# Optimization experiments

Measured on AMD Instinct MI355X. Metric: run time of the kernel, lower is better.

## Reference

```python
import jax, jax.numpy as jnp
import numpy as np

QMAX = 127.0          # int8 clip bound (symmetric, preserve-zero)
QDIV = 127.5          # AQT int8 scale divisor: 2**(bits-1) - 0.5


def _safe(s):
    # avoid div-by-zero for all-zero rows/cols
    return jnp.where(s == 0.0, 1.0, s)


def setup_inputs() -> dict:
    key = jax.random.key(0)
    k1, k2 = jax.random.split(key)
    lhs = jax.random.normal(k1, (8192, 4096), dtype=jnp.float32)
    rhs = jax.random.normal(k2, (4096, 4096), dtype=jnp.float32)
    return {"lhs": lhs, "rhs": rhs}


def reference(lhs, rhs):
    # --- dynamic symmetric int8 quantization (AQT abs-max calibration) ---
    # lhs: contract over axis 1 -> per-row scale [M, 1]
    s_l = _safe(jnp.max(jnp.abs(lhs), axis=1, keepdims=True) / QDIV)
    # rhs: contract over axis 0 -> per-column scale [1, N]
    s_r = _safe(jnp.max(jnp.abs(rhs), axis=0, keepdims=True) / QDIV)

    q_l = jnp.clip(jnp.round(lhs / s_l), -QMAX, QMAX).astype(jnp.int8)
    q_r = jnp.clip(jnp.round(rhs / s_r), -QMAX, QMAX).astype(jnp.int8)

    # --- integer matmul with int32 accumulation ---
    acc = jax.lax.dot_general(
        q_l, q_r,
        dimension_numbers=(((1,), (0,)), ((), ())),
        preferred_element_type=jnp.int32,
    )

    # --- dequantize: outer product of per-row / per-column scales ---
    return acc.astype(jnp.float32) * s_l * s_r
```

## Files before the change

### kernel.cpp

```cpp
#include <hip/hip_runtime.h>
#include <stdint.h>

#define M_DIM 8192
#define N_DIM 4096
#define K_DIM 4096
#define QMAXF 127.0f
#define QDIVF 127.5f

typedef int v4i __attribute__((ext_vector_type(4)));

typedef __attribute__((address_space(3))) void lds_void_t;
typedef __attribute__((address_space(1))) const void glb_void_t;

static __device__ __forceinline__ void load_lds16(const void* g, void* l) {
    __builtin_amdgcn_global_load_lds((glb_void_t*)g, (lds_void_t*)l, 16, 0, 0);
}

__global__ __launch_bounds__(256) void prep1_kernel(
        const float* __restrict__ lhs, const float* __restrict__ rhs,
        float* __restrict__ sL, unsigned* __restrict__ bits,
        int8_t* __restrict__ ql) {
    const int t = threadIdx.x;
    if (blockIdx.x < M_DIM) {
        const int row = blockIdx.x;
        const float4* rp = (const float4*)(lhs + (size_t)row * K_DIM);
        float4 v[4];
        float m = 0.0f;
#pragma unroll
        for (int i = 0; i < 4; ++i) {
            v[i] = rp[t + i * 256];
            m = fmaxf(m, fmaxf(fmaxf(fabsf(v[i].x), fabsf(v[i].y)),
                               fmaxf(fabsf(v[i].z), fabsf(v[i].w))));
        }
#pragma unroll
        for (int off = 32; off; off >>= 1) m = fmaxf(m, __shfl_down(m, off, 64));
        __shared__ float wmax[4];
        if ((t & 63) == 0) wmax[t >> 6] = m;
        __syncthreads();
        const float mm = fmaxf(fmaxf(wmax[0], wmax[1]), fmaxf(wmax[2], wmax[3]));
        float s = mm / QDIVF;
        s = (s == 0.0f) ? 1.0f : s;
        if (t == 0) sL[row] = s;
        unsigned* qo = (unsigned*)ql + (size_t)row * 1024;
#pragma unroll
        for (int i = 0; i < 4; ++i) {
            int q0 = (int)fminf(fmaxf(rintf(v[i].x / s), -QMAXF), QMAXF);
            int q1 = (int)fminf(fmaxf(rintf(v[i].y / s), -QMAXF), QMAXF);
            int q2 = (int)fminf(fmaxf(rintf(v[i].z / s), -QMAXF), QMAXF);
            int q3 = (int)fminf(fmaxf(rintf(v[i].w / s), -QMAXF), QMAXF);
            qo[t + i * 256] = (q0 & 255) | ((q1 & 255) << 8) | ((q2 & 255) << 16)
                            | ((unsigned)(q3 & 255) << 24);
        }
    } else {
        const int cb = blockIdx.x - M_DIM;
        const int col = (cb & 15) * 256 + t;
        const int r0 = (cb >> 4) * 64;
        float m = 0.0f;
#pragma unroll 4
        for (int r = 0; r < 64; ++r)
            m = fmaxf(m, fabsf(rhs[(size_t)(r0 + r) * N_DIM + col]));
        atomicMax(&bits[col], __float_as_uint(m));
    }
}

__global__ __launch_bounds__(256) void quant_rhs_t_kernel(
        const float* __restrict__ rhs, const unsigned* __restrict__ bits,
        float* __restrict__ sR, int8_t* __restrict__ qbT) {
    __shared__ __align__(16) int8_t lt[64][80];
    const int n0 = blockIdx.x * 64;
    const int k0 = blockIdx.y * 64;
    const int t = threadIdx.x;
    const int nloc = t & 63;
    const int kq = (t >> 6) * 16;
    float s = __uint_as_float(bits[n0 + nloc]) / QDIVF;
    s = (s == 0.0f) ? 1.0f : s;
    if (blockIdx.y == 0 && t < 64) {
        float ss = __uint_as_float(bits[n0 + t]) / QDIVF;
        sR[n0 + t] = (ss == 0.0f) ? 1.0f : ss;
    }
#pragma unroll
    for (int i = 0; i < 4; ++i) {
        unsigned pack = 0;
#pragma unroll
        for (int j = 0; j < 4; ++j) {
            int kk = kq + i * 4 + j;
            float x = rhs[(size_t)(k0 + kk) * N_DIM + n0 + nloc];
            int q = (int)fminf(fmaxf(rintf(x / s), -QMAXF), QMAXF);
            pack |= (unsigned)(q & 255) << (8 * j);
        }
        *(unsigned*)&lt[nloc][kq + i * 4] = pack;
    }
    __syncthreads();
    const int nn = t >> 2, ch = t & 3;
    v4i val = *(const v4i*)&lt[nn][ch * 16];
    *(v4i*)&qbT[(size_t)(n0 + nn) * K_DIM + k0 + ch * 16] = val;
}


#define BAR() do { asm volatile("" ::: "memory");          \
                   __builtin_amdgcn_s_barrier();           \
                   asm volatile("" ::: "memory"); } while (0)

#define VMCNT(N) asm volatile("s_waitcnt vmcnt(%0)" :: "n"(N) : "memory")

#define TILE(KT, BUF, S, VM) do {                                               \
    if (S) {                                                                    \
        load_lds16(gA0 + (size_t)((KT) + 2) * 64,                               \
                   lds + (((BUF) + 2) % 3) * 24576 + sdst);                     \
        load_lds16(gB0 + (size_t)((KT) + 2) * 64,                               \
                   lds + (((BUF) + 2) % 3) * 24576 + 8192 + sdst);              \
        load_lds16(gB0 + (size_t)128 * K_DIM + (size_t)((KT) + 2) * 64,         \
                   lds + (((BUF) + 2) % 3) * 24576 + 16384 + sdst);             \
    }                                                                           \
    _Pragma("unroll") for (int mm = 0; mm < 4; ++mm)                            \
        af[mm] = *(const v4i*)(lds + (BUF) * 24576 + aoff[mm]);                 \
    _Pragma("unroll") for (int nn = 0; nn < 4; ++nn)                            \
        bf[nn] = *(const v4i*)(lds + (BUF) * 24576 + boff[nn]);                 \
    __builtin_amdgcn_s_setprio(1);                                              \
    _Pragma("unroll") for (int mm = 0; mm < 4; ++mm)                            \
    _Pragma("unroll") for (int nn = 0; nn < 4; ++nn)                            \
        acc[mm][nn] = __builtin_amdgcn_mfma_i32_16x16x64_i8(                    \
            af[mm], bf[nn], acc[mm][nn], 0, 0, 0);                              \
    __builtin_amdgcn_s_setprio(0);                                              \
    VMCNT(VM);                                                                  \
    BAR();                                                                      \
} while (0)

__global__ __launch_bounds__(512, 4) void gemm_i8_kernel(
        const int8_t* __restrict__ qa, const int8_t* __restrict__ qbT,
        const float* __restrict__ sL, const float* __restrict__ sR,
        float* __restrict__ out) {
    __shared__ __align__(16) int8_t lds[73728];

    const int t = threadIdx.x;
    const int wave = t >> 6;
    const int lane = t & 63;

    const int bid = blockIdx.x;
    const int xcd = bid & 7;
    const int idx = bid >> 3;
    const int mt = (xcd >> 1) * 16 + (idx & 15);
    const int nt = (xcd & 1) * 8 + (idx >> 4);
    const int brow = mt * 128;
    const int bcol = nt * 256;

    const int wm = (wave >> 2) * 64;
    const int wn = (wave & 3) * 64;

    int aoff[4], boff[4];
#pragma unroll
    for (int m = 0; m < 4; ++m) {
        int row = wm + m * 16 + (lane & 15);
        aoff[m] = row * 64 + (((lane >> 4) ^ ((row >> 1) & 3)) * 16);
    }
#pragma unroll
    for (int n = 0; n < 4; ++n) {
        int row = wn + n * 16 + (lane & 15);
        boff[n] = 8192 + row * 64 + (((lane >> 4) ^ ((row >> 1) & 3)) * 16);
    }

    v4i acc[4][4];
#pragma unroll
    for (int m = 0; m < 4; ++m)
#pragma unroll
        for (int n = 0; n < 4; ++n) acc[m][n] = (v4i){0, 0, 0, 0};

    const int srow = t >> 2;
    const int lcA = (t & 3) ^ ((srow >> 1) & 3);
    const int8_t* gA0 = qa  + (size_t)(brow + srow) * K_DIM + lcA * 16;
    const int8_t* gB0 = qbT + (size_t)(bcol + srow) * K_DIM + lcA * 16;
    const int sdst = t * 16;

    v4i af[4], bf[4];

    load_lds16(gA0,                        lds + sdst);
    load_lds16(gB0,                        lds + 8192 + sdst);
    load_lds16(gB0 + (size_t)128 * K_DIM,  lds + 16384 + sdst);
    load_lds16(gA0 + 64,                       lds + 24576 + sdst);
    load_lds16(gB0 + 64,                       lds + 24576 + 8192 + sdst);
    load_lds16(gB0 + (size_t)128 * K_DIM + 64, lds + 24576 + 16384 + sdst);
    VMCNT(3);
    BAR();

    for (int kt = 0; kt < 60; kt += 3) {
        TILE(kt + 0, 0, 1, 3);
        TILE(kt + 1, 1, 1, 3);
        TILE(kt + 2, 2, 1, 3);
    }
    TILE(60, 0, 1, 3);
    TILE(61, 1, 1, 3);
    TILE(62, 2, 0, 0);
    TILE(63, 0, 0, 0);

    const int r4 = (lane >> 4) * 4;
    const int cc = lane & 15;
#pragma unroll
    for (int m = 0; m < 4; ++m) {
        const int grow0 = brow + wm + m * 16 + r4;
        const float s0 = sL[grow0 + 0];
        const float s1 = sL[grow0 + 1];
        const float s2 = sL[grow0 + 2];
        const float s3 = sL[grow0 + 3];
#pragma unroll
        for (int n = 0; n < 4; ++n) {
            const int gcol = bcol + wn + n * 16 + cc;
            const float sc = sR[gcol];
            float* o = out + (size_t)grow0 * N_DIM + gcol;
            o[0 * N_DIM] = (float)acc[m][n][0] * s0 * sc;
            o[1 * N_DIM] = (float)acc[m][n][1] * s1 * sc;
            o[2 * N_DIM] = (float)acc[m][n][2] * s2 * sc;
            o[3 * N_DIM] = (float)acc[m][n][3] * s3 * sc;
        }
    }
}

extern "C" void kernel_launch(void* const* d_in, const int* in_sizes, int n_in,
                              void* d_out, int out_size, void* d_ws, size_t ws_size,
                              hipStream_t stream) {
    const float* lhs = (const float*)d_in[0];
    const float* rhs = (const float*)d_in[1];
    float* out = (float*)d_out;

    uint8_t* ws = (uint8_t*)d_ws;
    int8_t* ql    = (int8_t*)ws;
    int8_t* qbT   = (int8_t*)(ws + 33554432);
    float* sL     = (float*)(ws + 50331648);
    float* sR     = (float*)(ws + 50331648 + 32768);
    unsigned* bits = (unsigned*)(ws + 50331648 + 32768 + 16384);

    hipMemsetAsync(bits, 0, N_DIM * sizeof(unsigned), stream);

    prep1_kernel<<<M_DIM + 1024, 256, 0, stream>>>(lhs, rhs, sL, bits, ql);
    quant_rhs_t_kernel<<<dim3(N_DIM / 64, K_DIM / 64), 256, 0, stream>>>(
        rhs, bits, sR, qbT);
    gemm_i8_kernel<<<dim3((M_DIM / 128) * (N_DIM / 256)), 512, 0, stream>>>(
        ql, qbT, sL, sR, out);
}
```

Before: 223.7 us.

## Enlarge GEMM tile to 256x256, load A fragments directly into registers

The int8 GEMM block tile grows from 128x256 to 256x256, and each wave now computes 64x128 with 32 accumulators. The A operand no longer goes through LDS: each wave loads its A fragments straight from global memory into double-buffered registers one k-step ahead. B stays staged in a 4-deep LDS ring via global_load_lds. This halves the grid and raises per-block reuse, in exchange for much higher register pressure (occupancy bound lowered to 2), and it relies on uncoalesced per-lane global A loads being hidden by the prefetch.

```diff
diff --git a/kernel.cpp b/kernel.cpp
--- a/kernel.cpp
+++ b/kernel.cpp
@@ -103,34 +103,34 @@
 
 #define VMCNT(N) asm volatile("s_waitcnt vmcnt(%0)" :: "n"(N) : "memory")
 
-#define TILE(KT, BUF, S, VM) do {                                               \
-    if (S) {                                                                    \
-        load_lds16(gA0 + (size_t)((KT) + 2) * 64,                               \
-                   lds + (((BUF) + 2) % 3) * 24576 + sdst);                     \
+#define TILE(KT, BUF, PAR, SA, SB, VM) do {                                     \
+    if (SA) {                                                                   \
+        _Pragma("unroll") for (int mm = 0; mm < 4; ++mm)                        \
+            an[(PAR) ^ 1][mm] = *(const v4i*)(pa[mm] + ((KT) + 1) * 64);        \
+    }                                                                           \
+    if (SB) {                                                                   \
         load_lds16(gB0 + (size_t)((KT) + 2) * 64,                               \
-                   lds + (((BUF) + 2) % 3) * 24576 + 8192 + sdst);              \
+                   lds + (((KT) + 2) & 3) * 16384 + sdst);                      \
         load_lds16(gB0 + (size_t)128 * K_DIM + (size_t)((KT) + 2) * 64,         \
-                   lds + (((BUF) + 2) % 3) * 24576 + 16384 + sdst);             \
+                   lds + (((KT) + 2) & 3) * 16384 + 8192 + sdst);               \
     }                                                                           \
-    _Pragma("unroll") for (int mm = 0; mm < 4; ++mm)                            \
-        af[mm] = *(const v4i*)(lds + (BUF) * 24576 + aoff[mm]);                 \
-    _Pragma("unroll") for (int nn = 0; nn < 4; ++nn)                            \
-        bf[nn] = *(const v4i*)(lds + (BUF) * 24576 + boff[nn]);                 \
+    _Pragma("unroll") for (int nn = 0; nn < 8; ++nn)                            \
+        bf[nn] = *(const v4i*)(lds + (BUF) * 16384 + boff[nn]);                 \
     __builtin_amdgcn_s_setprio(1);                                              \
     _Pragma("unroll") for (int mm = 0; mm < 4; ++mm)                            \
-    _Pragma("unroll") for (int nn = 0; nn < 4; ++nn)                            \
+    _Pragma("unroll") for (int nn = 0; nn < 8; ++nn)                            \
         acc[mm][nn] = __builtin_amdgcn_mfma_i32_16x16x64_i8(                    \
-            af[mm], bf[nn], acc[mm][nn], 0, 0, 0);                              \
+            an[PAR][mm], bf[nn], acc[mm][nn], 0, 0, 0);                         \
     __builtin_amdgcn_s_setprio(0);                                              \
     VMCNT(VM);                                                                  \
     BAR();                                                                      \
 } while (0)
 
-__global__ __launch_bounds__(512, 4) void gemm_i8_kernel(
+__global__ __launch_bounds__(512, 2) void gemm_i8_kernel(
         const int8_t* __restrict__ qa, const int8_t* __restrict__ qbT,
         const float* __restrict__ sL, const float* __restrict__ sR,
         float* __restrict__ out) {
-    __shared__ __align__(16) int8_t lds[73728];
+    __shared__ __align__(16) int8_t lds[65536];
 
     const int t = threadIdx.x;
     const int wave = t >> 6;
@@ -139,58 +139,59 @@
     const int bid = blockIdx.x;
     const int xcd = bid & 7;
     const int idx = bid >> 3;
-    const int mt = (xcd >> 1) * 16 + (idx & 15);
-    const int nt = (xcd & 1) * 8 + (idx >> 4);
-    const int brow = mt * 128;
+    const int mt = (xcd >> 1) * 8 + (idx >> 3);
+    const int nt = (xcd & 1) * 8 + (idx & 7);
+    const int brow = mt * 256;
     const int bcol = nt * 256;
 
-    const int wm = (wave >> 2) * 64;
-    const int wn = (wave & 3) * 64;
-
-    int aoff[4], boff[4];
-#pragma unroll
-    for (int m = 0; m < 4; ++m) {
-        int row = wm + m * 16 + (lane & 15);
-        aoff[m] = row * 64 + (((lane >> 4) ^ ((row >> 1) & 3)) * 16);
-    }
-#pragma unroll
-    for (int n = 0; n < 4; ++n) {
+    const int wm = (wave >> 1) * 64;
+    const int wn = (wave & 1) * 128;
+
+    const int8_t* pa[4];
+#pragma unroll
+    for (int m = 0; m < 4; ++m)
+        pa[m] = qa + (size_t)(brow + wm + m * 16 + (lane & 15)) * K_DIM
+                   + (lane >> 4) * 16;
+
+    int boff[8];
+#pragma unroll
+    for (int n = 0; n < 8; ++n) {
         int row = wn + n * 16 + (lane & 15);
-        boff[n] = 8192 + row * 64 + (((lane >> 4) ^ ((row >> 1) & 3)) * 16);
-    }
-
-    v4i acc[4][4];
+        boff[n] = row * 64 + (((lane >> 4) ^ ((row >> 1) & 3)) * 16);
+    }
+
+    v4i acc[4][8];
 #pragma unroll
     for (int m = 0; m < 4; ++m)
 #pragma unroll
-        for (int n = 0; n < 4; ++n) acc[m][n] = (v4i){0, 0, 0, 0};
+        for (int n = 0; n < 8; ++n) acc[m][n] = (v4i){0, 0, 0, 0};
 
     const int srow = t >> 2;
     const int lcA = (t & 3) ^ ((srow >> 1) & 3);
-    const int8_t* gA0 = qa  + (size_t)(brow + srow) * K_DIM + lcA * 16;
     const int8_t* gB0 = qbT + (size_t)(bcol + srow) * K_DIM + lcA * 16;
     const int sdst = t * 16;
 
-    v4i af[4], bf[4];
-
-    load_lds16(gA0,                        lds + sdst);
-    load_lds16(gB0,                        lds + 8192 + sdst);
-    load_lds16(gB0 + (size_t)128 * K_DIM,  lds + 16384 + sdst);
-    load_lds16(gA0 + 64,                       lds + 24576 + sdst);
-    load_lds16(gB0 + 64,                       lds + 24576 + 8192 + sdst);
-    load_lds16(gB0 + (size_t)128 * K_DIM + 64, lds + 24576 + 16384 + sdst);
-    VMCNT(3);
+    v4i an[2][4], bf[8];
+
+    load_lds16(gB0,                             lds + sdst);
+    load_lds16(gB0 + (size_t)128 * K_DIM,       lds + 8192 + sdst);
+    load_lds16(gB0 + 64,                        lds + 16384 + sdst);
+    load_lds16(gB0 + (size_t)128 * K_DIM + 64,  lds + 16384 + 8192 + sdst);
+#pragma unroll
+    for (int mm = 0; mm < 4; ++mm) an[0][mm] = *(const v4i*)(pa[mm]);
+    VMCNT(6);
     BAR();
 
-    for (int kt = 0; kt < 60; kt += 3) {
-        TILE(kt + 0, 0, 1, 3);
-        TILE(kt + 1, 1, 1, 3);
-        TILE(kt + 2, 2, 1, 3);
-    }
-    TILE(60, 0, 1, 3);
-    TILE(61, 1, 1, 3);
-    TILE(62, 2, 0, 0);
-    TILE(63, 0, 0, 0);
+    for (int kt = 0; kt < 60; kt += 4) {
+        TILE(kt + 0, 0, 0, 1, 1, 6);
+        TILE(kt + 1, 1, 1, 1, 1, 6);
+        TILE(kt + 2, 2, 0, 1, 1, 6);
+        TILE(kt + 3, 3, 1, 1, 1, 6);
+    }
+    TILE(60, 0, 0, 1, 1, 6);
+    TILE(61, 1, 1, 1, 1, 6);
+    TILE(62, 2, 0, 1, 0, 4);
+    TILE(63, 3, 1, 0, 0, 0);
 
     const int r4 = (lane >> 4) * 4;
     const int cc = lane & 15;
@@ -202,7 +203,7 @@
         const float s2 = sL[grow0 + 2];
         const float s3 = sL[grow0 + 3];
 #pragma unroll
-        for (int n = 0; n < 4; ++n) {
+        for (int n = 0; n < 8; ++n) {
             const int gcol = bcol + wn + n * 16 + cc;
             const float sc = sR[gcol];
             float* o = out + (size_t)grow0 * N_DIM + gcol;
@@ -233,6 +234,6 @@
     prep1_kernel<<<M_DIM + 1024, 256, 0, stream>>>(lhs, rhs, sL, bits, ql);
     quant_rhs_t_kernel<<<dim3(N_DIM / 64, K_DIM / 64), 256, 0, stream>>>(
         rhs, bits, sR, qbT);
-    gemm_i8_kernel<<<dim3((M_DIM / 128) * (N_DIM / 256)), 512, 0, stream>>>(
+    gemm_i8_kernel<<<dim3((M_DIM / 256) * (N_DIM / 256)), 512, 0, stream>>>(
         ql, qbT, sL, sR, out);
 }
```

Result: slower. 263.1 us (+17.6%).

## Enlarge GEMM tile to 256x256 with 8-phase interleaved LDS staging

Applied to the files above, without the earlier changes.

Doubles the block tile along M to 256x256, so each wave computes a 128x64 sub-tile with 32 accumulators. Each k-step is split into four phases, each issuing one quarter of the next stage's global-to-LDS loads before a chunk of MFMAs, with barriers between phases. The aim is more data reuse per byte loaded and better overlap of loads with compute. In exchange it uses more LDS (96KB) and more accumulator registers, lowers occupancy to 2 blocks, launches half as many blocks, and adds many extra barriers per k-step.

```diff
diff --git a/kernel.cpp b/kernel.cpp
--- a/kernel.cpp
+++ b/kernel.cpp
@@ -103,34 +103,51 @@
 
 #define VMCNT(N) asm volatile("s_waitcnt vmcnt(%0)" :: "n"(N) : "memory")
 
-#define TILE(KT, BUF, S, VM) do {                                               \
-    if (S) {                                                                    \
-        load_lds16(gA0 + (size_t)((KT) + 2) * 64,                               \
-                   lds + (((BUF) + 2) % 3) * 24576 + sdst);                     \
-        load_lds16(gB0 + (size_t)((KT) + 2) * 64,                               \
-                   lds + (((BUF) + 2) % 3) * 24576 + 8192 + sdst);              \
-        load_lds16(gB0 + (size_t)128 * K_DIM + (size_t)((KT) + 2) * 64,         \
-                   lds + (((BUF) + 2) % 3) * 24576 + 16384 + sdst);             \
-    }                                                                           \
+#define RD_A(BUF, MF) (*(const v4i*)(lds + (BUF) * 32768 + aoff[MF]))
+#define RD_B(BUF, NF) (*(const v4i*)(lds + (BUF) * 32768 + boff[NF]))
+
+#define STAGE_H(PTR, KT, OFF) \
+    load_lds16((PTR) + (size_t)(KT) * 64, lds + ((KT) % 3) * 32768 + (OFF) + sdst8)
+
+#define MFMA8(MB, NB)                                                           \
     _Pragma("unroll") for (int mm = 0; mm < 4; ++mm)                            \
-        af[mm] = *(const v4i*)(lds + (BUF) * 24576 + aoff[mm]);                 \
-    _Pragma("unroll") for (int nn = 0; nn < 4; ++nn)                            \
-        bf[nn] = *(const v4i*)(lds + (BUF) * 24576 + boff[nn]);                 \
-    __builtin_amdgcn_s_setprio(1);                                              \
-    _Pragma("unroll") for (int mm = 0; mm < 4; ++mm)                            \
-    _Pragma("unroll") for (int nn = 0; nn < 4; ++nn)                            \
-        acc[mm][nn] = __builtin_amdgcn_mfma_i32_16x16x64_i8(                    \
-            af[mm], bf[nn], acc[mm][nn], 0, 0, 0);                              \
-    __builtin_amdgcn_s_setprio(0);                                              \
-    VMCNT(VM);                                                                  \
+    _Pragma("unroll") for (int nn = 0; nn < 2; ++nn)                            \
+        acc[(MB) + mm][(NB) + nn] = __builtin_amdgcn_mfma_i32_16x16x64_i8(      \
+            af[mm], bf[(NB) + nn], acc[(MB) + mm][(NB) + nn], 0, 0, 0);
+
+#define TILE8(KT, BUF, S, VMLAST) do {                                          \
+                                                              \
+    _Pragma("unroll") for (int mm = 0; mm < 4; ++mm) af[mm] = RD_A(BUF, mm);    \
+    bf[0] = RD_B(BUF, 0); bf[1] = RD_B(BUF, 1);                                 \
+    if (S) STAGE_H(gA0, (KT) + 2, 0);                                           \
+    BAR();                                                                      \
+    __builtin_amdgcn_s_setprio(1); MFMA8(0, 0); __builtin_amdgcn_s_setprio(0);  \
+    BAR();                                                                      \
+                                                              \
+    bf[2] = RD_B(BUF, 2); bf[3] = RD_B(BUF, 3);                                 \
+    if (S) STAGE_H(gA1, (KT) + 2, 8192);                                        \
+    BAR();                                                                      \
+    __builtin_amdgcn_s_setprio(1); MFMA8(0, 2); __builtin_amdgcn_s_setprio(0);  \
+    BAR();                                                                      \
+                                                              \
+    _Pragma("unroll") for (int mm = 0; mm < 4; ++mm) af[mm] = RD_A(BUF, 4 + mm);\
+    if (S) STAGE_H(gB0, (KT) + 2, 16384);                                       \
+    BAR();                                                                      \
+    __builtin_amdgcn_s_setprio(1); MFMA8(4, 0); __builtin_amdgcn_s_setprio(0);  \
+    BAR();                                                                      \
+                                                              \
+    if (S) STAGE_H(gB1, (KT) + 2, 24576);                                       \
+    VMCNT(VMLAST);                                                              \
+    BAR();                                                                      \
+    __builtin_amdgcn_s_setprio(1); MFMA8(4, 2); __builtin_amdgcn_s_setprio(0);  \
     BAR();                                                                      \
 } while (0)
 
-__global__ __launch_bounds__(512, 4) void gemm_i8_kernel(
+__global__ __launch_bounds__(512, 2) void gemm_i8_kernel(
         const int8_t* __restrict__ qa, const int8_t* __restrict__ qbT,
         const float* __restrict__ sL, const float* __restrict__ sR,
         float* __restrict__ out) {
-    __shared__ __align__(16) int8_t lds[73728];
+    __shared__ __align__(16) int8_t lds[98304];
 
     const int t = threadIdx.x;
     const int wave = t >> 6;
@@ -139,63 +156,63 @@
     const int bid = blockIdx.x;
     const int xcd = bid & 7;
     const int idx = bid >> 3;
-    const int mt = (xcd >> 1) * 16 + (idx & 15);
-    const int nt = (xcd & 1) * 8 + (idx >> 4);
-    const int brow = mt * 128;
+    const int mt = (xcd >> 1) * 8 + (idx & 7);
+    const int nt = (xcd & 1) * 8 + (idx >> 3);
+    const int brow = mt * 256;
     const int bcol = nt * 256;
 
-    const int wm = (wave >> 2) * 64;
+    const int wm = (wave >> 2) * 128;
     const int wn = (wave & 3) * 64;
 
-    int aoff[4], boff[4];
-#pragma unroll
-    for (int m = 0; m < 4; ++m) {
+    int aoff[8], boff[4];
+#pragma unroll
+    for (int m = 0; m < 8; ++m) {
         int row = wm + m * 16 + (lane & 15);
         aoff[m] = row * 64 + (((lane >> 4) ^ ((row >> 1) & 3)) * 16);
     }
 #pragma unroll
     for (int n = 0; n < 4; ++n) {
         int row = wn + n * 16 + (lane & 15);
-        boff[n] = 8192 + row * 64 + (((lane >> 4) ^ ((row >> 1) & 3)) * 16);
-    }
-
-    v4i acc[4][4];
-#pragma unroll
-    for (int m = 0; m < 4; ++m)
+        boff[n] = 16384 + row * 64 + (((lane >> 4) ^ ((row >> 1) & 3)) * 16);
+    }
+
+    v4i acc[8][4];
+#pragma unroll
+    for (int m = 0; m < 8; ++m)
 #pragma unroll
         for (int n = 0; n < 4; ++n) acc[m][n] = (v4i){0, 0, 0, 0};
 
     const int srow = t >> 2;
     const int lcA = (t & 3) ^ ((srow >> 1) & 3);
     const int8_t* gA0 = qa  + (size_t)(brow + srow) * K_DIM + lcA * 16;
+    const int8_t* gA1 = gA0 + (size_t)128 * K_DIM;
     const int8_t* gB0 = qbT + (size_t)(bcol + srow) * K_DIM + lcA * 16;
-    const int sdst = t * 16;
+    const int8_t* gB1 = gB0 + (size_t)128 * K_DIM;
+    const int sdst8 = t * 16;
 
     v4i af[4], bf[4];
 
-    load_lds16(gA0,                        lds + sdst);
-    load_lds16(gB0,                        lds + 8192 + sdst);
-    load_lds16(gB0 + (size_t)128 * K_DIM,  lds + 16384 + sdst);
-    load_lds16(gA0 + 64,                       lds + 24576 + sdst);
-    load_lds16(gB0 + 64,                       lds + 24576 + 8192 + sdst);
-    load_lds16(gB0 + (size_t)128 * K_DIM + 64, lds + 24576 + 16384 + sdst);
-    VMCNT(3);
+    STAGE_H(gA0, 0, 0); STAGE_H(gA1, 0, 8192);
+    STAGE_H(gB0, 0, 16384); STAGE_H(gB1, 0, 24576);
+    STAGE_H(gA0, 1, 0); STAGE_H(gA1, 1, 8192);
+    STAGE_H(gB0, 1, 16384); STAGE_H(gB1, 1, 24576);
+    VMCNT(4);
     BAR();
 
     for (int kt = 0; kt < 60; kt += 3) {
-        TILE(kt + 0, 0, 1, 3);
-        TILE(kt + 1, 1, 1, 3);
-        TILE(kt + 2, 2, 1, 3);
-    }
-    TILE(60, 0, 1, 3);
-    TILE(61, 1, 1, 3);
-    TILE(62, 2, 0, 0);
-    TILE(63, 0, 0, 0);
+        TILE8(kt + 0, 0, 1, 4);
+        TILE8(kt + 1, 1, 1, 4);
+        TILE8(kt + 2, 2, 1, 4);
+    }
+    TILE8(60, 0, 1, 4);
+    TILE8(61, 1, 1, 4);
+    TILE8(62, 2, 0, 0);
+    TILE8(63, 0, 0, 0);
 
     const int r4 = (lane >> 4) * 4;
     const int cc = lane & 15;
 #pragma unroll
-    for (int m = 0; m < 4; ++m) {
+    for (int m = 0; m < 8; ++m) {
         const int grow0 = brow + wm + m * 16 + r4;
         const float s0 = sL[grow0 + 0];
         const float s1 = sL[grow0 + 1];
@@ -233,6 +250,6 @@
     prep1_kernel<<<M_DIM + 1024, 256, 0, stream>>>(lhs, rhs, sL, bits, ql);
     quant_rhs_t_kernel<<<dim3(N_DIM / 64, K_DIM / 64), 256, 0, stream>>>(
         rhs, bits, sR, qbT);
-    gemm_i8_kernel<<<dim3((M_DIM / 128) * (N_DIM / 256)), 512, 0, stream>>>(
+    gemm_i8_kernel<<<dim3((M_DIM / 256) * (N_DIM / 256)), 512, 0, stream>>>(
         ql, qbT, sL, sR, out);
 }
```

New measurement: 210.9 us. -5.7%, faster.
